# Performance work log

Hardware: AMD Instinct MI355X
Metric: run time of the kernel (lower is better)

The kernel has to match this reference:

```python
import jax, jax.numpy as jnp
import numpy as np

N, D_IN, D_EMB, K = 16384, 1024, 256, 1024
ALPHA, EPS = 0.01, 1e-5


def setup_inputs() -> dict:
    key = jax.random.key(0)
    ks = jax.random.split(key, 6)
    inp = jax.random.normal(ks[0], (N, D_IN), dtype=jnp.float32)
    W_send = jax.random.normal(ks[1], (D_IN, D_EMB), dtype=jnp.float32) / np.sqrt(D_IN)
    b_send = jnp.zeros((D_EMB,), dtype=jnp.float32)
    W_recv = jax.random.normal(ks[2], (D_EMB, D_IN), dtype=jnp.float32) / np.sqrt(D_EMB)
    b_recv = jnp.zeros((D_IN,), dtype=jnp.float32)
    codebook = jax.random.normal(ks[3], (K, D_EMB), dtype=jnp.float32)
    ema_vecs = codebook.copy()
    ema_size = jnp.zeros((K,), dtype=jnp.float32)
    return {"input": inp, "W_send": W_send, "b_send": b_send,
            "W_recv": W_recv, "b_recv": b_recv, "codebook": codebook,
            "ema_vecs": ema_vecs, "ema_size": ema_size}


def reference(input, W_send, b_send, W_recv, b_recv, codebook, ema_vecs, ema_size):
    sg = jax.lax.stop_gradient
    # send projection -> latent z  [N, D_EMB]
    z = input @ W_send + b_send
    # nearest-neighbor lookup: argmin_k ||e_k||^2 - 2 <z, e_k>
    sqr = jnp.sum(codebook * codebook, axis=1)          # [K]
    cov = jnp.einsum('nj,kj->nk', z, codebook)          # [N, K]
    codes = jnp.argmin(sqr - 2.0 * cov, axis=-1)        # [N] int
    # fetch embeddings (gather)
    vectors = codebook[codes]                            # [N, D_EMB]
    # mse losses, reduction='sum'
    embedding = jnp.sum((vectors - sg(z)) ** 2)
    commitment = jnp.sum((z - sg(vectors)) ** 2)
    # straight-through output
    emb_out = z + sg(vectors - z)
    # EMA accumulate (one-hot scatter == segment_sum)
    upd_vecs = jax.ops.segment_sum(z, codes, num_segments=K)              # [K, D_EMB]
    upd_size = jax.ops.segment_sum(jnp.ones((z.shape[0],), z.dtype), codes, num_segments=K)
    ema_vecs_new = ema_vecs + ALPHA * (upd_vecs - ema_vecs)
    ema_size_new = ema_size + ALPHA * (upd_size - ema_size)
    # EMA update (Laplace-smoothed centroid)
    n = jnp.sum(ema_size_new)
    coef = n / (n + K * EPS)
    size = coef * (ema_size_new + EPS)
    weight_new = ema_vecs_new / size[:, None]
    # empirical entropy of the codes in bits
    prob = jnp.bincount(codes, length=K).astype(jnp.float32) / codes.size
    ent = -jnp.sum(jnp.where(prob > 0, prob * jnp.log(prob), 0.0)) / jnp.log(2.0)
    # recv projection
    x = emb_out @ W_recv + b_recv
    return (x, codes, embedding, commitment, ent, ema_vecs_new, ema_size_new, weight_new)
```

## Files before the change

kernel.cpp:

```cpp
#include <hip/hip_runtime.h>
#include <math.h>

#define NROWS 16384
#define DIN   1024
#define DEMB  256
#define KC    1024
#define ALPHA 0.01f
#define EPSV  1e-5f
#define INV2048 4.8828125e-4f
#define CHUNK 32
#define COV_CHUNKS 8

typedef _Float16 f16;
typedef __attribute__((ext_vector_type(4)))  _Float16 f16x4;
typedef __attribute__((ext_vector_type(8)))  _Float16 f16x8;
typedef __attribute__((ext_vector_type(16))) float    f32x16;
typedef unsigned long long u64;

#define OFF_Z       0
#define OFF_R       4194304
#define OFF_SQR     5242880
#define OFF_ZH      5243904
#define OFF_ZL      7341056
#define OFF_WTH     9438208
#define OFF_WTL     9569280
#define OFF_CBH     9700352
#define OFF_CBL     9831424
#define OFF_KEYS    9962496
#define OFF_CODES   9995264
#define OFF_LIST    10011648
#define OFF_OFFS    10028032
#define OFF_UPD     10029056
#define OFF_HIST    10291200
#define OFF_CURSOR  10292224
#define OFF_LOSS    10293248
#define OFF_SIZE    10294288

#define OUT_X      0
#define OUT_CODES  16777216
#define OUT_EMB    16793600
#define OUT_COMMIT 16793601
#define OUT_ENT    16793602
#define OUT_EMAV   16793603
#define OUT_EMAS   17055747
#define OUT_W      17056771

__device__ __forceinline__ void split_f32(float x, f16& h, f16& l) {
    h = (f16)x;
    l = (f16)((x - (float)h) * 2048.0f);
}

__global__ __launch_bounds__(256) void prep_kernel(const float* __restrict__ W_send,
                                                   const float* __restrict__ W_recv,
                                                   const float* __restrict__ cb,
                                                   float* __restrict__ ws) {
    const int b = blockIdx.x;
    const int t = threadIdx.x;
    int* wsi = (int*)ws;

    if (b < 256) {
        f16* wth = (f16*)(ws + OFF_WTH);
        f16* wtl = (f16*)(ws + OFF_WTL);
        const int n = b;
        f16x4 h4, l4;
#pragma unroll
        for (int j = 0; j < 4; ++j) {
            int k = t * 4 + j;
            float x = W_send[(size_t)k * DEMB + n];
            f16 h, l; split_f32(x, h, l);
            h4[j] = h; l4[j] = l;
        }
        *(f16x4*)&wth[(size_t)n * DIN + t * 4] = h4;
        *(f16x4*)&wtl[(size_t)n * DIN + t * 4] = l4;
    } else if (b < 512) {
        f16* cbh = (f16*)(ws + OFF_CBH);
        f16* cbl = (f16*)(ws + OFF_CBL);
        int idx = ((b - 256) * 256 + t) * 4;
        float4 v = *(const float4*)&cb[idx];
        f16x4 h4, l4;
        f16 h, l;
        split_f32(v.x, h, l); h4[0] = h; l4[0] = l;
        split_f32(v.y, h, l); h4[1] = h; l4[1] = l;
        split_f32(v.z, h, l); h4[2] = h; l4[2] = l;
        split_f32(v.w, h, l); h4[3] = h; l4[3] = l;
        *(f16x4*)&cbh[idx] = h4;
        *(f16x4*)&cbl[idx] = l4;
    } else if (b < 768) {
        f16* wrh = (f16*)(ws + OFF_ZH);
        f16* wrl = (f16*)(ws + OFF_ZH + 131072);
        const int n = (b - 512) * 4 + (t >> 6);
        const int lane = t & 63;
        f16x4 h4, l4;
#pragma unroll
        for (int j = 0; j < 4; ++j) {
            int k = lane * 4 + j;
            float x = W_recv[(size_t)k * DIN + n];
            f16 h, l; split_f32(x, h, l);
            h4[j] = h; l4[j] = l;
        }
        *(f16x4*)&wrh[(size_t)n * DEMB + lane * 4] = h4;
        *(f16x4*)&wrl[(size_t)n * DEMB + lane * 4] = l4;
    } else if (b < 1024) {
        float* sqr = ws + OFF_SQR;
        const int k = (b - 768) * 4 + (t >> 6);
        const int lane = t & 63;
        float4 v = ((const float4*)cb)[k * 64 + lane];
        float s = v.x * v.x + v.y * v.y + v.z * v.z + v.w * v.w;
        for (int off = 32; off > 0; off >>= 1) s += __shfl_down(s, off, 64);
        if (lane == 0) sqr[k] = s;
    } else if (b < 1280) {
        float4 zed = make_float4(0.f, 0.f, 0.f, 0.f);
        *(float4*)&ws[OFF_UPD + (size_t)(b - 1024) * 1024 + t * 4] = zed;
    } else if (b == 1280) {
#pragma unroll
        for (int j = 0; j < 4; ++j) {
            wsi[OFF_HIST + t * 4 + j] = 0;
            wsi[OFF_CURSOR + t * 4 + j] = 0;
        }
        if (t < 16) ws[OFF_LOSS + t] = 0.f;
    } else {
        u64* keys = (u64*)(ws + OFF_KEYS);
        keys[(b - 1281) * 256 + t] = ~0ull;
    }
}

__global__ __launch_bounds__(512) void gemm1_mfma(const float* __restrict__ in,
                                                  const f16* __restrict__ wth,
                                                  const f16* __restrict__ wtl,
                                                  const float* __restrict__ bsend,
                                                  float* __restrict__ z,
                                                  f16* __restrict__ zh,
                                                  f16* __restrict__ zl) {
    __shared__ f16 sm[2 * 2 * 2 * 128 * 64];
    const int tid = threadIdx.x;
    const int wave = tid >> 6, lane = tid & 63;
    const int half = lane >> 5, l31 = lane & 31;
    const int wrow = wave >> 2, wcol = wave & 3;

    const int L = blockIdx.x;
    const int v = L >> 3;
    const int bx = v & 1;
    const int by = (L & 7) + 8 * (v >> 1);
    const int rowBase = by * 128;
    const int colBase = bx * 128;

    const int sr  = tid >> 2;
    const int skq = tid & 3;
    const int sr7 = sr & 7;

    f32x16 accm[2] = {};
    f32x16 accx[2] = {};

    auto stageB = [&](int buf, int ks) {
#pragma unroll
        for (int i = 0; i < 4; ++i) {
            const int q  = wave * 4 + i;
            const int hl = q >> 4;
            const int c  = (q & 15) * 8 + (lane >> 3);
            const int p  = lane & 7;
            const int s  = p ^ (c & 7);
            const f16* src = (hl ? wtl : wth)
                           + (size_t)(colBase + c) * DIN + ks + s * 8;
            f16* dst = sm + buf * 32768 + 16384 + q * 512 + lane * 8;
            __builtin_amdgcn_global_load_lds(
                (const __attribute__((address_space(1))) void*)src,
                (__attribute__((address_space(3))) void*)dst, 16, 0, 0);
        }
    };

    auto loadA = [&](int ks, float4* av) {
        const float* src = &in[(size_t)(rowBase + sr) * DIN + ks + skq * 16];
#pragma unroll
        for (int j = 0; j < 4; ++j) av[j] = ((const float4*)src)[j];
    };

    auto writeA = [&](int buf, const float4* av) {
        f16* Abase = sm + buf * 32768;
#pragma unroll
        for (int q = 0; q < 2; ++q) {
            f16x8 h8, l8;
#pragma unroll
            for (int j = 0; j < 2; ++j) {
                float4 v4 = av[q * 2 + j];
                f16 h, l;
                split_f32(v4.x, h, l); h8[j * 4 + 0] = h; l8[j * 4 + 0] = l;
                split_f32(v4.y, h, l); h8[j * 4 + 1] = h; l8[j * 4 + 1] = l;
                split_f32(v4.z, h, l); h8[j * 4 + 2] = h; l8[j * 4 + 2] = l;
                split_f32(v4.w, h, l); h8[j * 4 + 3] = h; l8[j * 4 + 3] = l;
            }
            const int s = skq * 2 + q;
            const int off = sr * 64 + ((s ^ sr7) << 3);
            *(f16x8*)&Abase[off] = h8;
            *(f16x8*)&Abase[8192 + off] = l8;
        }
    };

    auto compute = [&](int buf) {
        const f16* Ah = sm + buf * 32768;
        const f16* Al = Ah + 8192;
        const f16* Bh = Ah + 16384;
        const f16* Bl = Ah + 24576;
        const int c  = wcol * 32 + l31;
        const int c7 = c & 7;
#pragma unroll
        for (int t4 = 0; t4 < 4; ++t4) {
            const int s = t4 * 2 + half;
            f16x8 a_h[2], a_l[2];
#pragma unroll
            for (int rt = 0; rt < 2; ++rt) {
                const int r = wrow * 64 + rt * 32 + l31;
                const int off = r * 64 + ((s ^ (r & 7)) << 3);
                a_h[rt] = *(const f16x8*)&Ah[off];
                a_l[rt] = *(const f16x8*)&Al[off];
            }
            const int boff = c * 64 + ((s ^ c7) << 3);
            f16x8 b_h = *(const f16x8*)&Bh[boff];
            f16x8 b_l = *(const f16x8*)&Bl[boff];
#pragma unroll
            for (int rt = 0; rt < 2; ++rt) {
                accm[rt] = __builtin_amdgcn_mfma_f32_32x32x16_f16(a_h[rt], b_h, accm[rt], 0, 0, 0);
                accx[rt] = __builtin_amdgcn_mfma_f32_32x32x16_f16(a_h[rt], b_l, accx[rt], 0, 0, 0);
                accx[rt] = __builtin_amdgcn_mfma_f32_32x32x16_f16(a_l[rt], b_h, accx[rt], 0, 0, 0);
            }
        }
    };

    stageB(0, 0);
    {
        float4 av[4];
        loadA(0, av);
        writeA(0, av);
    }
    __syncthreads();

    int cur = 0;
    for (int step = 0; step < 16; ++step) {
        float4 av[4];
        const bool pf = (step + 1) < 16;
        if (pf) {
            stageB(cur ^ 1, (step + 1) * 64);
            loadA((step + 1) * 64, av);
        }
        compute(cur);
        if (pf) writeA(cur ^ 1, av);
        __syncthreads();
        cur ^= 1;
    }

#pragma unroll
    for (int rt = 0; rt < 2; ++rt) {
        const int col = colBase + wcol * 32 + l31;
        const float bb = bsend[col];
#pragma unroll
        for (int reg = 0; reg < 16; ++reg) {
            const int row = rowBase + wrow * 64 + rt * 32 + (reg & 3) + 8 * (reg >> 2) + 4 * half;
            const float zv = accm[rt][reg] + INV2048 * accx[rt][reg] + bb;
            const size_t o = (size_t)row * DEMB + col;
            z[o] = zv;
            f16 h = (f16)zv;
            zh[o] = h;
            zl[o] = (f16)((zv - (float)h) * 2048.0f);
        }
    }
}

__global__ __launch_bounds__(256, 2) void gemm2_mfma(const f16* __restrict__ cbh,
                                                     const f16* __restrict__ cbl,
                                                     const f16* __restrict__ wrh,
                                                     const f16* __restrict__ wrl,
                                                     float* __restrict__ R) {
    __shared__ f16 sm[16384];
    const int tid = threadIdx.x;
    const int wave = tid >> 6, lane = tid & 63;
    const int half = lane >> 5, l31 = lane & 31;
    const int wr = wave >> 1, wc = wave & 1;
    const int rowBase = blockIdx.y * 64;
    const int colBase = blockIdx.x * 64;

    f32x16 accm = {}, accx = {};

    for (int step = 0; step < 4; ++step) {
        const int ks = step * 64;
        __syncthreads();
#pragma unroll
        for (int i = 0; i < 8; ++i) {
            const int q   = wave * 8 + i;
            const int arr = q >> 3;
            const int grp = q & 7;
            const int r   = grp * 8 + (lane >> 3);
            const int p   = lane & 7;
            const int s   = p ^ (r & 7);
            const f16* basep = (arr == 0) ? cbh : (arr == 1) ? cbl
                             : (arr == 2) ? wrh : wrl;
            const int rowg = ((arr >= 2) ? colBase : rowBase) + r;
            const f16* src = basep + (size_t)rowg * DEMB + ks + s * 8;
            f16* dst = sm + arr * 4096 + grp * 512;
            __builtin_amdgcn_global_load_lds(
                (const __attribute__((address_space(1))) void*)src,
                (__attribute__((address_space(3))) void*)dst, 16, 0, 0);
        }
        __syncthreads();
#pragma unroll
        for (int t = 0; t < 4; ++t) {
            const int sgi = t * 2 + half;
            const int ar = wr * 32 + l31;
            const int bc = wc * 32 + l31;
            const int aoff = ar * 64 + ((sgi ^ (ar & 7)) << 3);
            const int boff = bc * 64 + ((sgi ^ (bc & 7)) << 3);
            f16x8 a_h = *(const f16x8*)&sm[aoff];
            f16x8 a_l = *(const f16x8*)&sm[4096 + aoff];
            f16x8 b_h = *(const f16x8*)&sm[8192 + boff];
            f16x8 b_l = *(const f16x8*)&sm[12288 + boff];
            accm = __builtin_amdgcn_mfma_f32_32x32x16_f16(a_h, b_h, accm, 0, 0, 0);
            accx = __builtin_amdgcn_mfma_f32_32x32x16_f16(a_h, b_l, accx, 0, 0, 0);
            accx = __builtin_amdgcn_mfma_f32_32x32x16_f16(a_l, b_h, accx, 0, 0, 0);
        }
    }

    const int col = colBase + wc * 32 + l31;
#pragma unroll
    for (int reg = 0; reg < 16; ++reg) {
        const int row = rowBase + wr * 32 + (reg & 3) + 8 * (reg >> 2) + 4 * half;
        R[(size_t)row * DIN + col] = accm[reg] + INV2048 * accx[reg];
    }
}

__device__ __forceinline__ void cov_stage(const f16* __restrict__ cbh,
                                          const f16* __restrict__ cbl,
                                          f16* sC, int buf, int codeBase,
                                          int wave, int lane) {
#pragma unroll
    for (int i = 0; i < 8; ++i) {
        const int seg = wave * 8 + i;
        const int hl  = seg >> 4;
        const int rp  = seg & 15;
        const int r   = rp * 2 + (lane >> 5);
        const f16* src = (hl ? cbl : cbh)
                       + (size_t)(codeBase + r) * DEMB
                       + (((lane & 31) ^ r) << 3);
        f16* dst = sC + (((buf << 1) + hl) * 32 + rp * 2) * DEMB;
        __builtin_amdgcn_global_load_lds(
            (const __attribute__((address_space(1))) void*)src,
            (__attribute__((address_space(3))) void*)dst,
            16, 0, 0);
    }
}

__global__ __launch_bounds__(256, 2) void cov_mfma_kernel(const f16* __restrict__ zh,
                                                          const f16* __restrict__ zl,
                                                          const f16* __restrict__ cbh,
                                                          const f16* __restrict__ cbl,
                                                          const float* __restrict__ sqr,
                                                          u64* __restrict__ keys) {
    __shared__ f16 sC[2 * 2 * 32 * DEMB];
    const int tid = threadIdx.x;
    const int wave = tid >> 6, lane = tid & 63;
    const int half = lane >> 5, l31 = lane & 31;

    const int L = blockIdx.x;
    const int v = L >> 3;
    const int bx = v & 3;
    const int by = (L & 7) + 8 * (v >> 2);

    const int rowBase = by * 128 + wave * 32;
    const int myRow = rowBase + l31;
    const int cb0 = bx * (COV_CHUNKS * 32);

    cov_stage(cbh, cbl, sC, 0, cb0, wave, lane);

    f16x8 a_h[16], a_l[16];
#pragma unroll
    for (int t = 0; t < 16; ++t) {
        size_t o = (size_t)myRow * DEMB + t * 16 + half * 8;
        a_h[t] = *(const f16x8*)&zh[o];
        a_l[t] = *(const f16x8*)&zl[o];
    }

    float runv[16];
    int   runc[16];
#pragma unroll
    for (int r = 0; r < 16; ++r) { runv[r] = 3.4e38f; runc[r] = 0; }

    for (int cc = 0; cc < COV_CHUNKS; ++cc) {
        __syncthreads();
        if (cc + 1 < COV_CHUNKS)
            cov_stage(cbh, cbl, sC, (cc + 1) & 1, cb0 + (cc + 1) * 32, wave, lane);

        const f16* Ch = sC + ((cc & 1) * 2 + 0) * 32 * DEMB;
        const f16* Cl = sC + ((cc & 1) * 2 + 1) * 32 * DEMB;

        f32x16 accm = {};
        f32x16 accx = {};
#pragma unroll
        for (int t = 0; t < 16; ++t) {
            const int seg = t * 2 + half;
            const int p = ((seg ^ l31) << 3);
            f16x8 b_h = *(const f16x8*)&Ch[l31 * DEMB + p];
            f16x8 b_l = *(const f16x8*)&Cl[l31 * DEMB + p];
            accm = __builtin_amdgcn_mfma_f32_32x32x16_f16(a_h[t], b_h, accm, 0, 0, 0);
            accx = __builtin_amdgcn_mfma_f32_32x32x16_f16(a_h[t], b_l, accx, 0, 0, 0);
            accx = __builtin_amdgcn_mfma_f32_32x32x16_f16(a_l[t], b_h, accx, 0, 0, 0);
        }

        const int code = cb0 + cc * 32 + l31;
        const float sqv = sqr[code];
#pragma unroll
        for (int r = 0; r < 16; ++r) {
            float s = sqv - 2.0f * (accm[r] + INV2048 * accx[r]);
            if (s < runv[r]) { runv[r] = s; runc[r] = code; }
        }
    }

#pragma unroll
    for (int r = 0; r < 16; ++r) {
        float v2 = runv[r]; int ci = runc[r];
        for (int off = 16; off > 0; off >>= 1) {
            float ov = __shfl_down(v2, off, 32);
            int   oc = __shfl_down(ci, off, 32);
            if (ov < v2 || (ov == v2 && oc < ci)) { v2 = ov; ci = oc; }
        }
        if (l31 == 0) {
            int row = rowBase + (r & 3) + 8 * (r >> 2) + 4 * half;
            unsigned ub = __float_as_uint(v2);
            ub = (ub & 0x80000000u) ? ~ub : (ub | 0x80000000u);
            u64 key = ((u64)ub << 32) | (unsigned)ci;
            atomicMin(&keys[row], key);
        }
    }
}

__global__ __launch_bounds__(256) void decode_kernel(const u64* __restrict__ keys,
                                                     int* __restrict__ codes,
                                                     float* __restrict__ out_codes,
                                                     int* __restrict__ hist) {
    int r = blockIdx.x * 256 + threadIdx.x;
    int c = (int)(keys[r] & 0xFFFFFFFFull);
    codes[r] = c;
    out_codes[r] = (float)c;
    atomicAdd(&hist[c], 1);
}

__global__ __launch_bounds__(1024) void prefix_kernel(const int* __restrict__ hist,
                                                      const float* __restrict__ ema_size,
                                                      int* __restrict__ offs,
                                                      float* __restrict__ size_ws,
                                                      float* __restrict__ out) {
    __shared__ int s[1024];
    __shared__ float rn[1024];
    __shared__ float re[1024];
    const int t = threadIdx.x;
    const int v = hist[t];
    s[t] = v;
    const float c = (float)v;
    const float es = ema_size[t];
    const float esn = es + ALPHA * (c - es);
    out[OUT_EMAS + t] = esn;
    const float p = c * (1.0f / (float)NROWS);
    rn[t] = esn;
    re[t] = (p > 0.f) ? p * logf(p) : 0.f;
    __syncthreads();
    for (int d = 1; d < 1024; d <<= 1) {
        int x = (t >= d) ? s[t - d] : 0;
        __syncthreads();
        s[t] += x;
        __syncthreads();
    }
    offs[t] = s[t] - v;
    for (int d = 512; d > 0; d >>= 1) {
        if (t < d) { rn[t] += rn[t + d]; re[t] += re[t + d]; }
        __syncthreads();
    }
    const float n = rn[0];
    const float coef = n / (n + (float)KC * EPSV);
    size_ws[t] = coef * (esn + EPSV);
    if (t == 0) out[OUT_ENT] = -re[0] / logf(2.0f);
}

__global__ __launch_bounds__(256) void fill_kernel(const int* __restrict__ codes,
                                                   const int* __restrict__ offs,
                                                   int* __restrict__ cursor,
                                                   int* __restrict__ list) {
    int r = blockIdx.x * 256 + threadIdx.x;
    int c = codes[r];
    int pos = offs[c] + atomicAdd(&cursor[c], 1);
    list[pos] = r;
}

__global__ __launch_bounds__(256) void upd_loss_kernel(const float* __restrict__ z,
                                                       const float* __restrict__ cb,
                                                       const int* __restrict__ list,
                                                       const int* __restrict__ codes,
                                                       float* __restrict__ upd,
                                                       float* __restrict__ loss,
                                                       float* __restrict__ out_losses) {
    __shared__ int srow[CHUNK];
    __shared__ int scode[CHUNK];
    const int tid = threadIdx.x;
    const int base = blockIdx.x * CHUNK;
    if (tid < CHUNK) {
        int r = list[base + tid];
        srow[tid] = r;
        scode[tid] = codes[r];
    }
    __syncthreads();

    int cur = scode[0];
    float cbv = cb[(size_t)cur * DEMB + tid];
    float acc = 0.f, lacc = 0.f;
    float zv = z[(size_t)srow[0] * DEMB + tid];
#pragma unroll 4
    for (int i = 0; i < CHUNK; ++i) {
        float znext = (i + 1 < CHUNK) ? z[(size_t)srow[i + 1] * DEMB + tid] : 0.f;
        int c = scode[i];
        if (c != cur) {
            atomicAdd(&upd[(size_t)cur * DEMB + tid], acc);
            acc = 0.f;
            cur = c;
            cbv = cb[(size_t)cur * DEMB + tid];
        }
        acc += zv;
        float d = zv - cbv;
        lacc += d * d;
        zv = znext;
    }
    atomicAdd(&upd[(size_t)cur * DEMB + tid], acc);

    __shared__ float red[256];
    red[tid] = lacc;
    __syncthreads();
    for (int s = 128; s > 0; s >>= 1) {
        if (tid < s) red[tid] += red[tid + s];
        __syncthreads();
    }
    if (tid == 0) {
        atomicAdd(loss, red[0]);
        __threadfence();
        int tk = atomicAdd((int*)(loss + 8), 1);
        if (tk == (int)gridDim.x - 1) {
            float l = atomicAdd(loss, 0.0f);
            out_losses[0] = l;
            out_losses[1] = l;
        }
    }
}

__global__ __launch_bounds__(256) void recv_kernel(const float* __restrict__ R,
                                                   const float* __restrict__ brecv,
                                                   const int* __restrict__ codes,
                                                   float* __restrict__ out) {
    const int n = blockIdx.x;
    const int t = threadIdx.x;
    const int code = codes[n];
    float4 r = ((const float4*)(R + (size_t)code * DIN))[t];
    float4 b = ((const float4*)brecv)[t];
    ((float4*)(out + (size_t)n * DIN))[t] =
        make_float4(r.x + b.x, r.y + b.y, r.z + b.z, r.w + b.w);
}

__global__ __launch_bounds__(256) void emav_kernel(const float* __restrict__ ema_vecs,
                                                   const float* __restrict__ upd,
                                                   const float* __restrict__ size_ws,
                                                   float* __restrict__ out) {
    int idx = blockIdx.x * 256 + threadIdx.x;
    float ev = ema_vecs[idx], uv = upd[idx];
    float evn = ev + ALPHA * (uv - ev);
    out[OUT_EMAV + idx] = evn;
    out[OUT_W + idx] = evn / size_ws[idx >> 8];
}

extern "C" void kernel_launch(void* const* d_in, const int* in_sizes, int n_in,
                              void* d_out, int out_size, void* d_ws, size_t ws_size,
                              hipStream_t stream) {
    const float* input    = (const float*)d_in[0];
    const float* W_send   = (const float*)d_in[1];
    const float* b_send   = (const float*)d_in[2];
    const float* W_recv   = (const float*)d_in[3];
    const float* b_recv   = (const float*)d_in[4];
    const float* codebook = (const float*)d_in[5];
    const float* ema_vecs = (const float*)d_in[6];
    const float* ema_size = (const float*)d_in[7];
    float* out = (float*)d_out;
    float* ws  = (float*)d_ws;
    int*   wsi = (int*)d_ws;

    f16* wth = (f16*)(ws + OFF_WTH);
    f16* wtl = (f16*)(ws + OFF_WTL);
    f16* cbh = (f16*)(ws + OFF_CBH);
    f16* cbl = (f16*)(ws + OFF_CBL);
    f16* zh  = (f16*)(ws + OFF_ZH);
    f16* zl  = (f16*)(ws + OFF_ZL);
    u64* keys = (u64*)(ws + OFF_KEYS);
    f16* wrh = (f16*)(ws + OFF_ZH);
    f16* wrl = (f16*)(ws + OFF_ZH + 131072);

    prep_kernel<<<1345, 256, 0, stream>>>(W_send, W_recv, codebook, ws);

    gemm2_mfma<<<dim3(DIN / 64, KC / 64), 256, 0, stream>>>(
        cbh, cbl, wrh, wrl, ws + OFF_R);

    gemm1_mfma<<<(DEMB / 128) * (NROWS / 128), 512, 0, stream>>>(
        input, wth, wtl, b_send, ws + OFF_Z, zh, zl);

    cov_mfma_kernel<<<(KC / (COV_CHUNKS * 32)) * (NROWS / 128), 256, 0, stream>>>(
        zh, zl, cbh, cbl, ws + OFF_SQR, keys);

    decode_kernel<<<NROWS / 256, 256, 0, stream>>>(
        keys, wsi + OFF_CODES, out + OUT_CODES, wsi + OFF_HIST);

    prefix_kernel<<<1, 1024, 0, stream>>>(
        wsi + OFF_HIST, ema_size, wsi + OFF_OFFS, ws + OFF_SIZE, out);

    fill_kernel<<<NROWS / 256, 256, 0, stream>>>(
        wsi + OFF_CODES, wsi + OFF_OFFS, wsi + OFF_CURSOR, wsi + OFF_LIST);

    upd_loss_kernel<<<NROWS / CHUNK, 256, 0, stream>>>(
        ws + OFF_Z, codebook, wsi + OFF_LIST, wsi + OFF_CODES,
        ws + OFF_UPD, ws + OFF_LOSS, out + OUT_EMB);

    recv_kernel<<<NROWS, 256, 0, stream>>>(
        ws + OFF_R, b_recv, wsi + OFF_CODES, out + OUT_X);

    emav_kernel<<<KC, 256, 0, stream>>>(
        ema_vecs, ws + OFF_UPD, ws + OFF_SIZE, out);
}
```

Measured before the change: 258.1 us.

## Split-K gemm2 with atomics and double-buffered LDS, fuse recv and EMA tail kernels

Measured after the change: 264.2 us. 2.3% more time.

```diff
diff --git a/kernel.cpp b/kernel.cpp
--- a/kernel.cpp
+++ b/kernel.cpp
@@ -118,9 +118,12 @@
             wsi[OFF_CURSOR + t * 4 + j] = 0;
         }
         if (t < 16) ws[OFF_LOSS + t] = 0.f;
-    } else {
+    } else if (b < 1345) {
         u64* keys = (u64*)(ws + OFF_KEYS);
         keys[(b - 1281) * 256 + t] = ~0ull;
+    } else {
+        float4 zed = make_float4(0.f, 0.f, 0.f, 0.f);
+        *(float4*)&ws[OFF_R + (size_t)(b - 1345) * 1024 + t * 4] = zed;
     }
 }
 
@@ -269,19 +272,22 @@
                                                      const f16* __restrict__ wrh,
                                                      const f16* __restrict__ wrl,
                                                      float* __restrict__ R) {
-    __shared__ f16 sm[16384];
+    __shared__ f16 sm[2 * 16384];
     const int tid = threadIdx.x;
     const int wave = tid >> 6, lane = tid & 63;
     const int half = lane >> 5, l31 = lane & 31;
     const int wr = wave >> 1, wc = wave & 1;
-    const int rowBase = blockIdx.y * 64;
-    const int colBase = blockIdx.x * 64;
+
+    const int L = blockIdx.x;
+    const int kz = L & 1;
+    const int tile = L >> 1;
+    const int rowBase = (tile >> 4) * 64;
+    const int colBase = (tile & 15) * 64;
+    const int ks0 = kz * 128;
 
     f32x16 accm = {}, accx = {};
 
-    for (int step = 0; step < 4; ++step) {
-        const int ks = step * 64;
-        __syncthreads();
+    auto stage = [&](int buf, int ks) {
 #pragma unroll
         for (int i = 0; i < 8; ++i) {
             const int q   = wave * 8 + i;
@@ -294,12 +300,18 @@
                              : (arr == 2) ? wrh : wrl;
             const int rowg = ((arr >= 2) ? colBase : rowBase) + r;
             const f16* src = basep + (size_t)rowg * DEMB + ks + s * 8;
-            f16* dst = sm + arr * 4096 + grp * 512;
+            f16* dst = sm + buf * 16384 + arr * 4096 + grp * 512;
             __builtin_amdgcn_global_load_lds(
                 (const __attribute__((address_space(1))) void*)src,
                 (__attribute__((address_space(3))) void*)dst, 16, 0, 0);
         }
+    };
+
+    stage(0, ks0);
+    for (int s = 0; s < 2; ++s) {
         __syncthreads();
+        if (s == 0) stage(1, ks0 + 64);
+        const f16* base = sm + s * 16384;
 #pragma unroll
         for (int t = 0; t < 4; ++t) {
             const int sgi = t * 2 + half;
@@ -307,10 +319,10 @@
             const int bc = wc * 32 + l31;
             const int aoff = ar * 64 + ((sgi ^ (ar & 7)) << 3);
             const int boff = bc * 64 + ((sgi ^ (bc & 7)) << 3);
-            f16x8 a_h = *(const f16x8*)&sm[aoff];
-            f16x8 a_l = *(const f16x8*)&sm[4096 + aoff];
-            f16x8 b_h = *(const f16x8*)&sm[8192 + boff];
-            f16x8 b_l = *(const f16x8*)&sm[12288 + boff];
+            f16x8 a_h = *(const f16x8*)&base[aoff];
+            f16x8 a_l = *(const f16x8*)&base[4096 + aoff];
+            f16x8 b_h = *(const f16x8*)&base[8192 + boff];
+            f16x8 b_l = *(const f16x8*)&base[12288 + boff];
             accm = __builtin_amdgcn_mfma_f32_32x32x16_f16(a_h, b_h, accm, 0, 0, 0);
             accx = __builtin_amdgcn_mfma_f32_32x32x16_f16(a_h, b_l, accx, 0, 0, 0);
             accx = __builtin_amdgcn_mfma_f32_32x32x16_f16(a_l, b_h, accx, 0, 0, 0);
@@ -321,7 +333,7 @@
 #pragma unroll
     for (int reg = 0; reg < 16; ++reg) {
         const int row = rowBase + wr * 32 + (reg & 3) + 8 * (reg >> 2) + 4 * half;
-        R[(size_t)row * DIN + col] = accm[reg] + INV2048 * accx[reg];
+        atomicAdd(&R[(size_t)row * DIN + col], accm[reg] + INV2048 * accx[reg]);
     }
 }
 
@@ -544,28 +556,28 @@
     }
 }
 
-__global__ __launch_bounds__(256) void recv_kernel(const float* __restrict__ R,
+__global__ __launch_bounds__(256) void tail_kernel(const float* __restrict__ R,
                                                    const float* __restrict__ brecv,
                                                    const int* __restrict__ codes,
-                                                   float* __restrict__ out) {
-    const int n = blockIdx.x;
-    const int t = threadIdx.x;
-    const int code = codes[n];
-    float4 r = ((const float4*)(R + (size_t)code * DIN))[t];
-    float4 b = ((const float4*)brecv)[t];
-    ((float4*)(out + (size_t)n * DIN))[t] =
-        make_float4(r.x + b.x, r.y + b.y, r.z + b.z, r.w + b.w);
-}
-
-__global__ __launch_bounds__(256) void emav_kernel(const float* __restrict__ ema_vecs,
+                                                   const float* __restrict__ ema_vecs,
                                                    const float* __restrict__ upd,
                                                    const float* __restrict__ size_ws,
                                                    float* __restrict__ out) {
-    int idx = blockIdx.x * 256 + threadIdx.x;
-    float ev = ema_vecs[idx], uv = upd[idx];
-    float evn = ev + ALPHA * (uv - ev);
-    out[OUT_EMAV + idx] = evn;
-    out[OUT_W + idx] = evn / size_ws[idx >> 8];
+    const int b = blockIdx.x;
+    const int t = threadIdx.x;
+    if (b < NROWS) {
+        const int code = codes[b];
+        float4 r = ((const float4*)(R + (size_t)code * DIN))[t];
+        float4 bb = ((const float4*)brecv)[t];
+        ((float4*)(out + OUT_X + (size_t)b * DIN))[t] =
+            make_float4(r.x + bb.x, r.y + bb.y, r.z + bb.z, r.w + bb.w);
+    } else {
+        const int idx = (b - NROWS) * 256 + t;
+        float ev = ema_vecs[idx], uv = upd[idx];
+        float evn = ev + ALPHA * (uv - ev);
+        out[OUT_EMAV + idx] = evn;
+        out[OUT_W + idx] = evn / size_ws[idx >> 8];
+    }
 }
 
 extern "C" void kernel_launch(void* const* d_in, const int* in_sizes, int n_in,
@@ -593,9 +605,9 @@
     f16* wrh = (f16*)(ws + OFF_ZH);
     f16* wrl = (f16*)(ws + OFF_ZH + 131072);
 
-    prep_kernel<<<1345, 256, 0, stream>>>(W_send, W_recv, codebook, ws);
-
-    gemm2_mfma<<<dim3(DIN / 64, KC / 64), 256, 0, stream>>>(
+    prep_kernel<<<2369, 256, 0, stream>>>(W_send, W_recv, codebook, ws);
+
+    gemm2_mfma<<<512, 256, 0, stream>>>(
         cbh, cbl, wrh, wrl, ws + OFF_R);
 
     gemm1_mfma<<<(DEMB / 128) * (NROWS / 128), 512, 0, stream>>>(
@@ -617,9 +629,7 @@
         ws + OFF_Z, codebook, wsi + OFF_LIST, wsi + OFF_CODES,
         ws + OFF_UPD, ws + OFF_LOSS, out + OUT_EMB);
 
-    recv_kernel<<<NROWS, 256, 0, stream>>>(
-        ws + OFF_R, b_recv, wsi + OFF_CODES, out + OUT_X);
-
-    emav_kernel<<<KC, 256, 0, stream>>>(
-        ema_vecs, ws + OFF_UPD, ws + OFF_SIZE, out);
-}
+    tail_kernel<<<NROWS + 1024, 256, 0, stream>>>(
+        ws + OFF_R, b_recv, wsi + OFF_CODES, ema_vecs,
+        ws + OFF_UPD, ws + OFF_SIZE, out);
+}
```
